# Performance work log

Hardware: AMD Instinct MI355X
Metric: run time of the kernel (lower is better)

Reference implementation:

```python
import jax, jax.numpy as jnp
import numpy as np

SPATIAL = [(56, 100), (28, 50), (14, 25), (7, 13)]
L_TOT = sum(h * w for h, w in SPATIAL)  # 7441
IMG_H, IMG_W = 448.0, 800.0
HH, NLEV, NPTS = 8, 4, 4
C, FFN = 256, 1024
PC = [-54.0, -54.0, -5.0, 54.0, 54.0, 3.0]
GRID_XY = 1080 // 8


def mlp2(x, w1, b1, w2, b2):
    return jnp.maximum(x @ w1 + b1, 0.0) @ w2 + b2


def ln(x):
    m = x.mean(-1, keepdims=True)
    v = ((x - m) ** 2).mean(-1, keepdims=True)
    return (x - m) * jax.lax.rsqrt(v + 1e-5)


def bilinear_sample(feat, loc):
    # feat [h,w,D]; loc [N,2] normalized to [0,1]; zero padding, align_corners=False
    h, w = feat.shape[0], feat.shape[1]
    x = loc[:, 0] * w - 0.5
    y = loc[:, 1] * h - 0.5
    x0f = jnp.floor(x); y0f = jnp.floor(y)
    wx = (x - x0f)[:, None]; wy = (y - y0f)[:, None]
    x0 = x0f.astype(jnp.int32); y0 = y0f.astype(jnp.int32)
    def g(xi, yi):
        inb = ((xi >= 0) & (xi < w) & (yi >= 0) & (yi < h))[:, None]
        return feat[jnp.clip(yi, 0, h - 1), jnp.clip(xi, 0, w - 1)] * inb
    return (g(x0, y0) * (1 - wx) * (1 - wy) + g(x0 + 1, y0) * wx * (1 - wy)
            + g(x0, y0 + 1) * (1 - wx) * wy + g(x0 + 1, y0 + 1) * wx * wy)


def setup_inputs() -> dict:
    key = jax.random.key(0)
    ks = jax.random.split(key, 40)
    B, V, P = 4, 6, 200
    f = jnp.float32
    def w(i, shape, s=0.05):
        return jax.random.normal(ks[i], shape, f) * s
    inp = {
        'img_query_feat': jax.random.normal(ks[1], (B, C, P), f),
        'img_query_pos': jax.random.uniform(ks[2], (B, P, 3), dtype=f),
        'img_query_view_mask': jax.random.randint(ks[3], (B, P, V), 0, 2).astype(jnp.int32),
        'img_feats_stack': jax.random.normal(ks[4], (B, V, C, L_TOT), f),
        'normal_img_feats_pos_stack': jax.random.normal(ks[5], (L_TOT, 2), f),
        'lidar2img_rt': jnp.eye(4, dtype=f) + 0.01 * jax.random.normal(ks[0], (B, V, 4, 4), f),
        'lidar2cam_r': jnp.broadcast_to(jnp.eye(3, dtype=f), (B, V, 3, 3)) + 0.01 * jax.random.normal(ks[6], (B, V, 3, 3), f),
        'lidar2cam_t': jax.random.normal(ks[7], (B, V, 3), f),
        'qpos_w1': w(8, (3, C)), 'qpos_b1': jnp.zeros((C,), f),
        'qpos_w2': w(9, (C, C)), 'qpos_b2': jnp.zeros((C,), f),
        'kpos_w1': w(10, (6, C)), 'kpos_b1': jnp.zeros((C,), f),
        'kpos_w2': w(11, (C, C)), 'kpos_b2': jnp.zeros((C,), f),
        'sa_wq': w(12, (C, C)), 'sa_wk': w(13, (C, C)),
        'sa_wv': w(14, (C, C)), 'sa_wo': w(15, (C, C)),
        'dv_w': w(16, (C, C)),
        'doff_w': w(17, (C, HH * NLEV * NPTS * 2)), 'doff_b': jnp.zeros((HH * NLEV * NPTS * 2,), f),
        'dattn_w': w(18, (C, HH * NLEV * NPTS)), 'dattn_b': jnp.zeros((HH * NLEV * NPTS,), f),
        'dout_w': w(19, (C, C)),
        'ffn_w1': w(20, (C, FFN)), 'ffn_b1': jnp.zeros((FFN,), f),
        'ffn_w2': w(21, (FFN, C)), 'ffn_b2': jnp.zeros((C,), f),
        'pred_w1': w(22, (C, C)), 'pred_b1': jnp.zeros((C,), f),
        'pred_w2': w(23, (C, 3)), 'pred_b2': jnp.zeros((3,), f),
    }
    return inp


def reference(img_query_feat, img_query_pos, img_query_view_mask, img_feats_stack,
              normal_img_feats_pos_stack, lidar2img_rt, lidar2cam_r, lidar2cam_t,
              qpos_w1, qpos_b1, qpos_w2, qpos_b2, kpos_w1, kpos_b1, kpos_w2, kpos_b2,
              sa_wq, sa_wk, sa_wv, sa_wo, dv_w, doff_w, doff_b, dattn_w, dattn_b, dout_w,
              ffn_w1, ffn_b1, ffn_w2, ffn_b2, pred_w1, pred_b1, pred_w2, pred_b2):
    B, V, _, L = img_feats_stack.shape
    P = img_query_feat.shape[-1]
    Dh = C // HH

    # key 3D positions: denormalize -> backproject via inv(lidar2img) -> append cam center
    pos2d = jax.nn.sigmoid(normal_img_feats_pos_stack) * jnp.array([IMG_W, IMG_H], jnp.float32)
    pos4 = jnp.concatenate([pos2d, jnp.ones((L, 2), pos2d.dtype)], -1)  # [L,4]
    inv_rt = jnp.linalg.inv(lidar2img_rt)                               # [B,V,4,4]
    key3d = jnp.einsum('bvij,lj->bvli', inv_rt, pos4)[..., :3]          # [B,V,L,3]
    cam_t = -jnp.einsum('bvji,bvj->bvi', lidar2cam_r, lidar2cam_t)      # [B,V,3]
    key_pos6 = jnp.concatenate([key3d, jnp.broadcast_to(cam_t[:, :, None], key3d.shape)], -1)
    kpos_emb = mlp2(key_pos6, kpos_w1, kpos_b1, kpos_w2, kpos_b2)       # [B,V,L,C]
    qpos_emb = mlp2(img_query_pos, qpos_w1, qpos_b1, qpos_w2, qpos_b2)  # [B,P,C]

    # per-view normalized reference points from lidar->image projection
    qpad = jnp.concatenate([img_query_pos, jnp.ones((B, P, 1), img_query_pos.dtype)], -1)
    proj = jnp.einsum('bvij,bpj->bvpi', lidar2img_rt, qpad)
    ref = (proj[..., :2] / proj[..., 2:3]) / jnp.array([IMG_W, IMG_H], jnp.float32)  # [B,V,P,2]

    # on-image mask; views with <=1 query are skipped (as in original)
    mv = jnp.transpose(img_query_view_mask > 0, (0, 2, 1))  # [B,V,P]
    mv = mv & (mv.sum(-1, keepdims=True) > 1)

    # self attention among on-image queries (shared qkv, per-view key mask)
    x = jnp.transpose(img_query_feat, (0, 2, 1))  # [B,P,C]
    xq = x + qpos_emb
    q = (xq @ sa_wq).reshape(B, P, HH, Dh)
    k = (xq @ sa_wk).reshape(B, P, HH, Dh)
    v = (x @ sa_wv).reshape(B, P, HH, Dh)
    logits = jnp.einsum('bqhd,bkhd->bhqk', q, k) / np.sqrt(Dh).astype(np.float32)
    logits = logits[:, None] + jnp.where(mv[:, :, None, None, :], 0.0, -1e9)  # [B,V,HH,P,P]
    attn = jax.nn.softmax(logits, axis=-1)
    sa = jnp.einsum('bvhqk,bkhd->bvqhd', attn, v).reshape(B, V, P, C) @ sa_wo
    x1 = ln(x[:, None] + sa)  # [B,V,P,C]

    # multi-scale deformable cross attention
    vals = ((jnp.transpose(img_feats_stack, (0, 1, 3, 2)) + kpos_emb) @ dv_w).reshape(B, V, L, HH, Dh)
    q2 = x1 + qpos_emb[:, None]
    off = (q2 @ doff_w + doff_b).reshape(B, V, P, HH, NLEV, NPTS, 2)
    aw = jax.nn.softmax((q2 @ dattn_w + dattn_b).reshape(B, V, P, HH, NLEV * NPTS), -1)
    aw = aw.reshape(B, V, P, HH, NLEV, NPTS)
    wh = jnp.array([[float(w_), float(h_)] for (h_, w_) in SPATIAL], jnp.float32)  # [NLEV,2]
    loc = ref[:, :, :, None, None, None, :] + off / wh[:, None, :]
    out = jnp.zeros((B, V, P, HH, Dh), x.dtype)
    start = 0
    for l, (h_, w_) in enumerate(SPATIAL):
        feat_l = vals[:, :, start:start + h_ * w_]
        start += h_ * w_
        feat_l = jnp.transpose(feat_l.reshape(B, V, h_, w_, HH, Dh), (0, 1, 4, 2, 3, 5)).reshape(B * V * HH, h_, w_, Dh)
        loc_l = jnp.transpose(loc[:, :, :, :, l], (0, 1, 3, 2, 4, 5)).reshape(B * V * HH, P * NPTS, 2)
        s = jax.vmap(bilinear_sample)(feat_l, loc_l).reshape(B, V, HH, P, NPTS, Dh)
        out = out + jnp.einsum('bvhpnd,bvphn->bvphd', s, aw[:, :, :, :, l])
    x2 = ln(x1 + out.reshape(B, V, P, C) @ dout_w)
    x3 = ln(x2 + mlp2(x2, ffn_w1, ffn_b1, ffn_w2, ffn_b2))  # [B,V,P,C]

    # masked scatter-accumulate across views, count-normalized
    mk = mv[..., None].astype(x.dtype)            # [B,V,P,1]
    fused = (x3 * mk).sum(1) / (mk.sum(1) + 1e-4)  # [B,P,C]
    img_query_feat_out = jnp.transpose(fused, (0, 2, 1))

    # prediction head: center refinement + BEV normalization
    center = mlp2(fused, pred_w1, pred_b1, pred_w2, pred_b2) + img_query_pos  # [B,P,3]
    img_query_pos_out = jax.lax.stop_gradient(center)
    cx = (center[..., 0] - PC[0]) / (PC[3] - PC[0]) * GRID_XY
    cy = (center[..., 1] - PC[1]) / (PC[4] - PC[1]) * GRID_XY
    center_bev = jnp.stack([cx, cy], -1)
    img_query_pos_bev = jax.lax.stop_gradient(center_bev)
    height = jnp.transpose(center[..., 2:3], (0, 2, 1))
    center_out = jnp.transpose(center_bev, (0, 2, 1))
    return img_query_feat_out, img_query_pos_out, img_query_pos_bev, center_out, height
```

## Files before the change

### kernel.cpp

```cpp
#include <hip/hip_runtime.h>
#include <hip/hip_bf16.h>
#include <cstdint>
#include <cstddef>

using bf16 = __hip_bfloat16;
#define DEVFN static __device__ __forceinline__

constexpr int B = 4, V = 6, P = 200, C = 256, HH = 8, Dh = 32, NLEV = 4, NPTS = 4, FFN = 1024;
constexpr int L = 7441;
constexpr int BV = B * V, BP = B * P, BVP = B * V * P, BVL = B * V * L;
constexpr float IMG_W = 800.f, IMG_H = 448.f;

__constant__ int cLH[4] = {56, 28, 14, 7};
__constant__ int cLW[4] = {100, 50, 25, 13};
__constant__ int cLS[4] = {0, 5600, 7000, 7350};

constexpr size_t IRT   = 0;
constexpr size_t CAMT  = IRT + (size_t)BV * 16;
constexpr size_t MFLAG = CAMT + (size_t)BV * 3;
constexpr size_t Xo    = MFLAG + BV;
constexpr size_t QPOSo = Xo + (size_t)BP * C;
constexpr size_t Qo    = QPOSo + (size_t)BP * C;
constexpr size_t Ko    = Qo + (size_t)BP * C;
constexpr size_t VVo   = Ko + (size_t)BP * C;
constexpr size_t LOGo  = VVo + (size_t)BP * C;
constexpr size_t SAo   = LOGo + (size_t)B * HH * P * P;
constexpr size_t X1o   = SAo + (size_t)BVP * C;
constexpr size_t REFo  = X1o + (size_t)BVP * C;
constexpr size_t OFFo  = REFo + (size_t)BVP * 2;
constexpr size_t AWo   = OFFo + (size_t)BVP * 256;
constexpr size_t OUTSo = AWo + (size_t)BVP * 128;
constexpr size_t X2o   = OUTSo + (size_t)BVP * C;
constexpr size_t X3o   = X2o + (size_t)BVP * C;
constexpr size_t FUSEDo= X3o + (size_t)BVP * C;
constexpr size_t B2DVo = FUSEDo + (size_t)BP * C;
constexpr size_t WS_FLOATS = B2DVo + 256;
constexpr size_t VALS_BYTE_OFF = ((WS_FLOATS * 4 + 255) / 256) * 256;
constexpr size_t VALS_ELEMS = (size_t)BVL * C;

constexpr size_t KW2NB_O = 0;
constexpr size_t DVWT_O  = 65536;
constexpr size_t WOT_O   = 131072;
constexpr size_t DOUTT_O = 196608;
constexpr size_t OAWT_O  = 262144;
constexpr size_t QKVT_O  = 360448;
constexpr size_t W1T_O   = 753664;
constexpr size_t W2T_O   = 1015808;
constexpr size_t HIDB_O  = 1277952;
constexpr size_t KDVT_O  = HIDB_O;

constexpr size_t O0 = 0;
constexpr size_t O1 = O0 + (size_t)B * C * P;
constexpr size_t O2 = O1 + (size_t)B * P * 3;
constexpr size_t O3 = O2 + (size_t)B * P * 2;
constexpr size_t O4 = O3 + (size_t)B * 2 * P;

DEVFN float tof(bf16 x) { return __bfloat162float(x); }
DEVFN bf16  tobf(float x) { return __float2bfloat16(x); }

typedef __attribute__((ext_vector_type(8))) short short8;
typedef __attribute__((ext_vector_type(4))) float floatx4;

DEVFN float blockReduceSum(float v, float* red) {
    int j = threadIdx.x;
    __syncthreads();
    red[j] = v; __syncthreads();
    for (int s = 128; s > 0; s >>= 1) { if (j < s) red[j] += red[j + s]; __syncthreads(); }
    return red[0];
}

DEVFN float dotK(const float* __restrict__ s, const float* __restrict__ W, int j, int N, int K) {
    float acc = 0.f;
    for (int k = 0; k < K; k += 4) {
        float4 h = *(const float4*)(s + k);
        acc += h.x * W[(size_t)(k + 0) * N + j];
        acc += h.y * W[(size_t)(k + 1) * N + j];
        acc += h.z * W[(size_t)(k + 2) * N + j];
        acc += h.w * W[(size_t)(k + 3) * N + j];
    }
    return acc;
}

__global__ __launch_bounds__(64) void k_setup(const float* rt, const float* l2cr, const float* l2ct,
                                              const int* maskin, float* ws) {
    int t = threadIdx.x;
    if (t >= BV) return;
    float m[16], inv[16];
    for (int i = 0; i < 16; i++) m[i] = rt[t * 16 + i];
    inv[0]  =  m[5]*m[10]*m[15] - m[5]*m[11]*m[14] - m[9]*m[6]*m[15] + m[9]*m[7]*m[14] + m[13]*m[6]*m[11] - m[13]*m[7]*m[10];
    inv[4]  = -m[4]*m[10]*m[15] + m[4]*m[11]*m[14] + m[8]*m[6]*m[15] - m[8]*m[7]*m[14] - m[12]*m[6]*m[11] + m[12]*m[7]*m[10];
    inv[8]  =  m[4]*m[9]*m[15]  - m[4]*m[11]*m[13] - m[8]*m[5]*m[15] + m[8]*m[7]*m[13] + m[12]*m[5]*m[11] - m[12]*m[7]*m[9];
    inv[12] = -m[4]*m[9]*m[14]  + m[4]*m[10]*m[13] + m[8]*m[5]*m[14] - m[8]*m[6]*m[13] - m[12]*m[5]*m[10] + m[12]*m[6]*m[9];
    inv[1]  = -m[1]*m[10]*m[15] + m[1]*m[11]*m[14] + m[9]*m[2]*m[15] - m[9]*m[3]*m[14] - m[13]*m[2]*m[11] + m[13]*m[3]*m[10];
    inv[5]  =  m[0]*m[10]*m[15] - m[0]*m[11]*m[14] - m[8]*m[2]*m[15] + m[8]*m[3]*m[14] + m[12]*m[2]*m[11] - m[12]*m[3]*m[10];
    inv[9]  = -m[0]*m[9]*m[15]  + m[0]*m[11]*m[13] + m[8]*m[1]*m[15] - m[8]*m[3]*m[13] - m[12]*m[1]*m[11] + m[12]*m[3]*m[9];
    inv[13] =  m[0]*m[9]*m[14]  - m[0]*m[10]*m[13] - m[8]*m[1]*m[14] + m[8]*m[2]*m[13] + m[12]*m[1]*m[10] - m[12]*m[2]*m[9];
    inv[2]  =  m[1]*m[6]*m[15]  - m[1]*m[7]*m[14]  - m[5]*m[2]*m[15] + m[5]*m[3]*m[14] + m[13]*m[2]*m[7]  - m[13]*m[3]*m[6];
    inv[6]  = -m[0]*m[6]*m[15]  + m[0]*m[7]*m[14]  + m[4]*m[2]*m[15] - m[4]*m[3]*m[14] - m[12]*m[2]*m[7]  + m[12]*m[3]*m[6];
    inv[10] =  m[0]*m[5]*m[15]  - m[0]*m[7]*m[13]  - m[4]*m[1]*m[15] + m[4]*m[3]*m[13] + m[12]*m[1]*m[7]  - m[12]*m[3]*m[5];
    inv[14] = -m[0]*m[5]*m[14]  + m[0]*m[6]*m[13]  + m[4]*m[1]*m[14] - m[4]*m[2]*m[13] - m[12]*m[1]*m[6]  + m[12]*m[2]*m[5];
    inv[3]  = -m[1]*m[6]*m[11]  + m[1]*m[7]*m[10]  + m[5]*m[2]*m[11] - m[5]*m[3]*m[10] - m[9]*m[2]*m[7]   + m[9]*m[3]*m[6];
    inv[7]  =  m[0]*m[6]*m[11]  - m[0]*m[7]*m[10]  - m[4]*m[2]*m[11] + m[4]*m[3]*m[10] + m[8]*m[2]*m[7]   - m[8]*m[3]*m[6];
    inv[11] = -m[0]*m[5]*m[11]  + m[0]*m[7]*m[9]   + m[4]*m[1]*m[11] - m[4]*m[3]*m[9]  - m[8]*m[1]*m[7]   + m[8]*m[3]*m[5];
    inv[15] =  m[0]*m[5]*m[10]  - m[0]*m[6]*m[9]   - m[4]*m[1]*m[10] + m[4]*m[2]*m[9]  + m[8]*m[1]*m[6]   - m[8]*m[2]*m[5];
    float det = m[0]*inv[0] + m[1]*inv[4] + m[2]*inv[8] + m[3]*inv[12];
    float rd = 1.f / det;
    for (int i = 0; i < 16; i++) ws[IRT + t * 16 + i] = inv[i] * rd;
    float r9[9], tv[3];
    for (int i = 0; i < 9; i++) r9[i] = l2cr[t * 9 + i];
    for (int i = 0; i < 3; i++) tv[i] = l2ct[t * 3 + i];
    for (int i = 0; i < 3; i++)
        ws[CAMT + t * 3 + i] = -(r9[0 * 3 + i] * tv[0] + r9[1 * 3 + i] * tv[1] + r9[2 * 3 + i] * tv[2]);
    int b = t / V, v = t % V, cnt = 0;
    for (int p = 0; p < P; p++) cnt += (maskin[(b * P + p) * V + v] > 0) ? 1 : 0;
    ws[MFLAG + t] = (cnt > 1) ? 1.f : 0.f;
}

__global__ __launch_bounds__(256) void k_wprep_all(
        const float* kw2, const float* dvw, const float* wo, const float* dw,
        const float* offw, const float* attw, const float* wq, const float* wk, const float* wv,
        const float* w1, const float* w2, bf16* wb) {
    int bid = blockIdx.x, t = threadIdx.x;
    if (bid < 1024) {
        int reg = bid >> 8, n = bid & 255;
        if (reg == 0) {
            wb[(size_t)n * 256 + t] = tobf(kw2[(size_t)n * 256 + t]);
        } else {
            const float* src = (reg == 1) ? dvw : (reg == 2) ? wo : dw;
            wb[(size_t)reg * 65536 + (size_t)n * 256 + t] = tobf(src[(size_t)t * 256 + n]);
        }
    } else if (bid < 1408) {
        int n = bid - 1024;
        float v = (n < 256) ? offw[(size_t)t * 256 + n] : attw[(size_t)t * 128 + (n - 256)];
        wb[OAWT_O + (size_t)n * 256 + t] = tobf(v);
    } else if (bid < 2176) {
        int n = bid - 1408;
        bf16* dst = wb + QKVT_O + (size_t)n * 512;
        float v0 = (n < 256) ? wq[(size_t)t * 256 + n] : (n < 512) ? wk[(size_t)t * 256 + (n - 256)]
                                                                   : wv[(size_t)t * 256 + (n - 512)];
        dst[t] = tobf(v0);
        float v1 = (n < 256) ? wq[(size_t)t * 256 + n] : (n < 512) ? wk[(size_t)t * 256 + (n - 256)] : 0.f;
        dst[t + 256] = tobf(v1);
    } else if (bid < 3200) {
        int n = bid - 2176;
        wb[W1T_O + (size_t)n * 256 + t] = tobf(w1[(size_t)t * 1024 + n]);
    } else {
        int n = bid - 3200;
        bf16* dst = wb + W2T_O + (size_t)n * 1024;
        for (int kk = 0; kk < 4; kk++)
            dst[t + kk * 256] = tobf(w2[(size_t)(t + kk * 256) * 256 + n]);
    }
}

constexpr int GAST = 264;
__global__ __launch_bounds__(256) void k_wfuse(const bf16* __restrict__ dvwT, const bf16* __restrict__ kw2nb,
                                               const float* __restrict__ b2, bf16* __restrict__ kdvT,
                                               float* ws) {
    __shared__ __align__(16) bf16 As[32 * GAST];
    int row0 = blockIdx.x * 32;
    int t = threadIdx.x;
    for (int rr = 0; rr < 32; rr++)
        As[rr * GAST + t] = dvwT[(size_t)(row0 + rr) * 256 + t];
    __syncthreads();
    int wave = t >> 6, lane = t & 63, quad = lane >> 4, l15 = lane & 15;
    int n0 = wave * 64;
    floatx4 acc[2][4];
    #pragma unroll
    for (int i = 0; i < 2; i++)
        #pragma unroll
        for (int nt = 0; nt < 4; nt++) acc[i][nt] = (floatx4){0.f, 0.f, 0.f, 0.f};
    for (int kk = 0; kk < 8; kk++) {
        short8 a0 = *(const short8*)&As[l15 * GAST + kk * 32 + quad * 8];
        short8 a1 = *(const short8*)&As[(16 + l15) * GAST + kk * 32 + quad * 8];
        #pragma unroll
        for (int nt = 0; nt < 4; nt++) {
            short8 bf = *(const short8*)&kw2nb[(size_t)(n0 + nt * 16 + l15) * 256 + kk * 32 + quad * 8];
            acc[0][nt] = __builtin_amdgcn_mfma_f32_16x16x32_bf16(a0, bf, acc[0][nt], 0, 0, 0);
            acc[1][nt] = __builtin_amdgcn_mfma_f32_16x16x32_bf16(a1, bf, acc[1][nt], 0, 0, 0);
        }
    }
    #pragma unroll
    for (int i = 0; i < 2; i++)
        #pragma unroll
        for (int nt = 0; nt < 4; nt++) {
            int col = n0 + nt * 16 + l15;
            int rl = i * 16 + quad * 4;
            #pragma unroll
            for (int u = 0; u < 4; u++)
                kdvT[(size_t)(row0 + rl + u) * 256 + col] = tobf(acc[i][nt][u]);
        }
    {
        int r = t >> 3, pp = t & 7;
        float s = 0.f;
        for (int n = pp * 32; n < pp * 32 + 32; n++)
            s += tof(As[r * GAST + n]) * b2[n];
        s += __shfl_down(s, 4, 8);
        s += __shfl_down(s, 2, 8);
        s += __shfl_down(s, 1, 8);
        if (pp == 0) ws[B2DVo + row0 + r] = s;
    }
}

__global__ __launch_bounds__(256) void k_qpos(const float* qfeat, const float* qposin,
                                              const float* w1, const float* b1, const float* w2, const float* b2,
                                              float* ws) {
    int row = blockIdx.x, j = threadIdx.x;
    int b = row / P, p = row % P;
    __shared__ __align__(16) float pos[4];
    __shared__ __align__(16) float hid[C];
    if (j < 3) pos[j] = qposin[row * 3 + j];
    __syncthreads();
    float h = b1[j] + pos[0] * w1[0 * C + j] + pos[1] * w1[1 * C + j] + pos[2] * w1[2 * C + j];
    hid[j] = fmaxf(h, 0.f);
    __syncthreads();
    float acc = b2[j] + dotK(hid, w2, j, C, C);
    ws[QPOSo + (size_t)row * C + j] = acc;
    ws[Xo + (size_t)row * C + j] = qfeat[((size_t)b * C + j) * P + p];
}

constexpr int AST2 = 520;
__global__ __launch_bounds__(256) void k_qkv_mfma(const bf16* __restrict__ qkvT, float* ws) {
    __shared__ __align__(16) bf16 As[16 * AST2];
    int row0 = blockIdx.x * 16;
    int t = threadIdx.x;
    for (int rr = 0; rr < 16; rr++) {
        As[rr * AST2 + t]       = tobf(ws[Xo + (size_t)(row0 + rr) * C + t]);
        As[rr * AST2 + 256 + t] = tobf(ws[QPOSo + (size_t)(row0 + rr) * C + t]);
    }
    __syncthreads();
    int wave = t >> 6, lane = t & 63, quad = lane >> 4, l15 = lane & 15;
    int n0 = wave * 192;
    floatx4 acc[12];
    #pragma unroll
    for (int nt = 0; nt < 12; nt++) acc[nt] = (floatx4){0.f, 0.f, 0.f, 0.f};
    for (int kk = 0; kk < 16; kk++) {
        short8 a = *(const short8*)&As[l15 * AST2 + kk * 32 + quad * 8];
        #pragma unroll
        for (int nt = 0; nt < 12; nt++) {
            short8 bf = *(const short8*)&qkvT[(size_t)(n0 + nt * 16 + l15) * 512 + kk * 32 + quad * 8];
            acc[nt] = __builtin_amdgcn_mfma_f32_16x16x32_bf16(a, bf, acc[nt], 0, 0, 0);
        }
    }
    #pragma unroll
    for (int nt = 0; nt < 12; nt++) {
        int n = n0 + nt * 16 + l15;
        int which = n >> 8, c = n & 255;
        size_t dst = (which == 0) ? Qo : (which == 1) ? Ko : VVo;
        int row = row0 + quad * 4;
        #pragma unroll
        for (int u = 0; u < 4; u++)
            ws[dst + (size_t)(row + u) * C + c] = acc[nt][u];
    }
}

__global__ __launch_bounds__(256) void k_logits(float* ws) {
    int bid = blockIdx.x;
    int qi = bid % P, h = (bid / P) % HH, b = bid / (P * HH);
    int j = threadIdx.x;
    __shared__ __align__(16) float qf[Dh];
    if (j < Dh) qf[j] = ws[Qo + ((size_t)(b * P + qi)) * C + h * Dh + j];
    __syncthreads();
    if (j < P) {
        const float* kp = ws + Ko + ((size_t)(b * P + j)) * C + h * Dh;
        float acc = 0.f;
        for (int d = 0; d < Dh; d += 4) {
            float4 kv = *(const float4*)(kp + d);
            float4 qv = *(const float4*)(qf + d);
            acc += kv.x * qv.x + kv.y * qv.y + kv.z * qv.z + kv.w * qv.w;
        }
        ws[LOGo + (size_t)bid * P + j] = acc * 0.17677669529663687f;
    }
}

__global__ __launch_bounds__(256) void k_sattn(const int* maskin, float* ws) {
    int bid = blockIdx.x;
    int qi = bid % P, h = (bid / P) % HH, v = (bid / (P * HH)) % V, b = bid / (P * HH * V);
    int j = threadIdx.x;
    __shared__ float attn[256];
    __shared__ float red[256];
    __shared__ float rw[8];
    float flag = ws[MFLAG + b * V + v];
    float val = -1e30f;
    if (j < P) {
        float lg = ws[LOGo + ((size_t)(b * HH + h) * P + qi) * P + j];
        bool mk = (flag > 0.5f) && (maskin[(b * P + j) * V + v] > 0);
        val = lg + (mk ? 0.f : -1e9f);
    }
    int wv = j >> 6;
    float m = val;
    #pragma unroll
    for (int off = 32; off > 0; off >>= 1) m = fmaxf(m, __shfl_xor(m, off, 64));
    if ((j & 63) == 0) rw[wv] = m;
    __syncthreads();
    m = fmaxf(fmaxf(rw[0], rw[1]), fmaxf(rw[2], rw[3]));
    float e = (j < P) ? __expf(val - m) : 0.f;
    float s = e;
    #pragma unroll
    for (int off = 32; off > 0; off >>= 1) s += __shfl_xor(s, off, 64);
    if ((j & 63) == 0) rw[4 + wv] = s;
    __syncthreads();
    s = (rw[4] + rw[5]) + (rw[6] + rw[7]);
    attn[j] = e / s;
    __syncthreads();
    int d = j & 31, c = j >> 5;
    const float* vvp = ws + VVo + (size_t)b * P * C + h * Dh + d;
    float acc = 0.f;
    for (int kk = c * 25; kk < c * 25 + 25; ++kk) acc += attn[kk] * vvp[(size_t)kk * C];
    red[j] = acc; __syncthreads();
    if (j < Dh) {
        float s2 = 0.f;
        for (int c2 = 0; c2 < 8; c2++) s2 += red[c2 * 32 + j];
        ws[SAo + ((size_t)((b * V + v) * P + qi)) * C + h * Dh + j] = s2;
    }
}

constexpr int OST = 260;
__global__ __launch_bounds__(256) void k_lngemm(const bf16* __restrict__ WT,
        float* ws, size_t aOff, size_t residOff, int residMode, size_t dstOff) {
    __shared__ __align__(16) bf16 As[32 * GAST];
    __shared__ __align__(16) float Os[32 * OST];
    __shared__ float redw[4][8][2];
    __shared__ float mv[8][2];
    int row0 = blockIdx.x * 32;
    int t = threadIdx.x;
    for (int rr = 0; rr < 32; rr++)
        As[rr * GAST + t] = tobf(ws[aOff + (size_t)(row0 + rr) * C + t]);
    __syncthreads();
    int wave = t >> 6, lane = t & 63, quad = lane >> 4, l15 = lane & 15;
    int n0 = wave * 64;
    floatx4 acc[2][4];
    #pragma unroll
    for (int i = 0; i < 2; i++)
        #pragma unroll
        for (int nt = 0; nt < 4; nt++) acc[i][nt] = (floatx4){0.f, 0.f, 0.f, 0.f};
    for (int kk = 0; kk < 8; kk++) {
        short8 a0 = *(const short8*)&As[l15 * GAST + kk * 32 + quad * 8];
        short8 a1 = *(const short8*)&As[(16 + l15) * GAST + kk * 32 + quad * 8];
        #pragma unroll
        for (int nt = 0; nt < 4; nt++) {
            short8 bf = *(const short8*)&WT[(size_t)(n0 + nt * 16 + l15) * 256 + kk * 32 + quad * 8];
            acc[0][nt] = __builtin_amdgcn_mfma_f32_16x16x32_bf16(a0, bf, acc[0][nt], 0, 0, 0);
            acc[1][nt] = __builtin_amdgcn_mfma_f32_16x16x32_bf16(a1, bf, acc[1][nt], 0, 0, 0);
        }
    }
    #pragma unroll
    for (int i = 0; i < 2; i++)
        #pragma unroll
        for (int nt = 0; nt < 4; nt++) {
            int col = n0 + nt * 16 + l15;
            int rl = i * 16 + quad * 4;
            #pragma unroll
            for (int u = 0; u < 4; u++) Os[(rl + u) * OST + col] = acc[i][nt][u];
        }
    __syncthreads();
    int lane2 = t & 63, wv = t >> 6;
    for (int g = 0; g < 4; g++) {
        float rv[8];
        #pragma unroll
        for (int r = 0; r < 8; r++) {
            int grow = row0 + g * 8 + r;
            int ridx = residMode ? ((grow / (P * V)) * P + grow % P) : grow;
            rv[r] = Os[(g * 8 + r) * OST + t] + ws[residOff + (size_t)ridx * C + t];
        }
        #pragma unroll
        for (int r = 0; r < 8; r++) {
            float s = rv[r], q = rv[r] * rv[r];
            for (int off = 32; off > 0; off >>= 1) {
                s += __shfl_down(s, off, 64);
                q += __shfl_down(q, off, 64);
            }
            if (lane2 == 0) { redw[wv][r][0] = s; redw[wv][r][1] = q; }
        }
        __syncthreads();
        if (t < 8) {
            float s = redw[0][t][0] + redw[1][t][0] + redw[2][t][0] + redw[3][t][0];
            float q = redw[0][t][1] + redw[1][t][1] + redw[2][t][1] + redw[3][t][1];
            float mean = s * (1.f / C);
            float var = q * (1.f / C) - mean * mean;
            mv[t][0] = mean; mv[t][1] = rsqrtf(var + 1e-5f);
        }
        __syncthreads();
        #pragma unroll
        for (int r = 0; r < 8; r++) {
            int grow = row0 + g * 8 + r;
            ws[dstOff + (size_t)grow * C + t] = (rv[r] - mv[r][0]) * mv[r][1];
        }
        __syncthreads();
    }
}

__global__ __launch_bounds__(256) void k_ref(const float* qposin, const float* rt, float* ws) {
    int tid = blockIdx.x * 256 + threadIdx.x;
    if (tid >= BVP) return;
    int p = tid % P, v = (tid / P) % V, b = tid / (P * V);
    float p0 = qposin[(b * P + p) * 3 + 0];
    float p1 = qposin[(b * P + p) * 3 + 1];
    float p2 = qposin[(b * P + p) * 3 + 2];
    const float* m = rt + (size_t)(b * V + v) * 16;
    float pr[3];
    for (int i = 0; i < 3; i++)
        pr[i] = m[i * 4 + 0] * p0 + m[i * 4 + 1] * p1 + m[i * 4 + 2] * p2 + m[i * 4 + 3];
    ws[REFo + (size_t)tid * 2 + 0] = pr[0] / pr[2] / IMG_W;
    ws[REFo + (size_t)tid * 2 + 1] = pr[1] / pr[2] / IMG_H;
}

constexpr int OAWST = 392;
__global__ __launch_bounds__(256) void k_offaw_mfma(const bf16* __restrict__ oawT,
        const float* __restrict__ ob, const float* __restrict__ ab, float* ws) {
    __shared__ __align__(16) bf16 As[32 * GAST];
    __shared__ __align__(16) float Os[32 * OAWST];
    int row0 = blockIdx.x * 32;
    int t = threadIdx.x;
    for (int rr = 0; rr < 32; rr++) {
        int grow = row0 + rr;
        int ridx = (grow / (P * V)) * P + grow % P;
        As[rr * GAST + t] = tobf(ws[X1o + (size_t)grow * C + t] + ws[QPOSo + (size_t)ridx * C + t]);
    }
    __syncthreads();
    int wave = t >> 6, lane = t & 63, quad = lane >> 4, l15 = lane & 15;
    int n0 = wave * 96;
    floatx4 acc[2][6];
    #pragma unroll
    for (int i = 0; i < 2; i++)
        #pragma unroll
        for (int nt = 0; nt < 6; nt++) acc[i][nt] = (floatx4){0.f, 0.f, 0.f, 0.f};
    for (int kk = 0; kk < 8; kk++) {
        short8 a0 = *(const short8*)&As[l15 * GAST + kk * 32 + quad * 8];
        short8 a1 = *(const short8*)&As[(16 + l15) * GAST + kk * 32 + quad * 8];
        #pragma unroll
        for (int nt = 0; nt < 6; nt++) {
            short8 bf = *(const short8*)&oawT[(size_t)(n0 + nt * 16 + l15) * 256 + kk * 32 + quad * 8];
            acc[0][nt] = __builtin_amdgcn_mfma_f32_16x16x32_bf16(a0, bf, acc[0][nt], 0, 0, 0);
            acc[1][nt] = __builtin_amdgcn_mfma_f32_16x16x32_bf16(a1, bf, acc[1][nt], 0, 0, 0);
        }
    }
    #pragma unroll
    for (int i = 0; i < 2; i++)
        #pragma unroll
        for (int nt = 0; nt < 6; nt++) {
            int col = n0 + nt * 16 + l15;
            int rl = i * 16 + quad * 4;
            #pragma unroll
            for (int u = 0; u < 4; u++) Os[(rl + u) * OAWST + col] = acc[i][nt][u];
        }
    __syncthreads();
    float obv = ob[t];
    for (int r = 0; r < 32; r++)
        ws[OFFo + (size_t)(row0 + r) * 256 + t] = Os[r * OAWST + t] + obv;
    {
        int r = t >> 3, g = t & 7;
        const float* lg = &Os[r * OAWST + 256 + g * 16];
        float mx = -1e30f;
        #pragma unroll
        for (int i = 0; i < 16; i++) mx = fmaxf(mx, lg[i] + ab[g * 16 + i]);
        float s = 0.f;
        float ex[16];
        #pragma unroll
        for (int i = 0; i < 16; i++) { ex[i] = __expf(lg[i] + ab[g * 16 + i] - mx); s += ex[i]; }
        float rs = 1.f / s;
        #pragma unroll
        for (int i = 0; i < 16; i++)
            ws[AWo + (size_t)(row0 + r) * 128 + g * 16 + i] = ex[i] * rs;
    }
}

constexpr int VROWS = 64;
constexpr int ASTR = C + 8;
constexpr int NVT = (L + VROWS - 1) / VROWS;

DEVFN int swidx(int r, int c) {
    return r * ASTR + ((c & 7) | ((((c >> 3) ^ ((r >> 3) & 7))) << 3));
}
DEVFN int swblk(int r, int cb) {
    return r * ASTR + (((cb ^ ((r >> 3) & 7))) << 3);
}

__global__ __launch_bounds__(256, 4) void k_vals_mfma(
        const float* __restrict__ npos, const float* __restrict__ feats,
        const float* __restrict__ kw1, const float* __restrict__ kb1,
        const bf16* __restrict__ kdvT, const bf16* __restrict__ dvwT,
        const float* __restrict__ ws, bf16* __restrict__ vals) {
    __shared__ __align__(16) bf16 As[VROWS * ASTR];
    __shared__ float kp6s[VROWS][8];
    __shared__ float b2s[C];
    int bv = blockIdx.y;
    int l0 = blockIdx.x * VROWS;
    int t = threadIdx.x;
    bool full = (l0 + VROWS <= L);

    float4 fb1[8];
    if (full) {
        #pragma unroll
        for (int rnd = 0; rnd < 8; rnd++) {
            int c = rnd * 16 + (t >> 4), ql = (t & 15) * 4;
            fb1[rnd] = *(const float4*)&feats[((size_t)bv * C + c) * L + l0 + ql];
        }
    }
    b2s[t] = ws[B2DVo + t];
    if (t < VROWS) {
        int l = min(l0 + t, L - 1);
        float sx = 1.f / (1.f + __expf(-npos[l * 2 + 0])) * IMG_W;
        float sy = 1.f / (1.f + __expf(-npos[l * 2 + 1])) * IMG_H;
        const float* inv = ws + IRT + (size_t)bv * 16;
        #pragma unroll
        for (int i = 0; i < 3; i++)
            kp6s[t][i] = inv[i * 4 + 0] * sx + inv[i * 4 + 1] * sy + inv[i * 4 + 2] + inv[i * 4 + 3];
        #pragma unroll
        for (int i = 0; i < 3; i++) kp6s[t][3 + i] = ws[CAMT + (size_t)bv * 3 + i];
    }
    __syncthreads();
    {
        float w1j[6];
        #pragma unroll
        for (int i = 0; i < 6; i++) w1j[i] = kw1[i * C + t];
        float bb = kb1[t];
        for (int r = 0; r < VROWS; r++) {
            float h = bb;
            #pragma unroll
            for (int i = 0; i < 6; i++) h += kp6s[r][i] * w1j[i];
            As[swidx(r, t)] = tobf(fmaxf(h, 0.f));
        }
    }
    __syncthreads();
    int wave = t >> 6, lane = t & 63;
    int quad = lane >> 4, l15 = lane & 15;
    int mh = (wave >> 1) * 32;
    int nh = (wave & 1) * 128;
    floatx4 acc[2][8];
    #pragma unroll
    for (int i = 0; i < 2; i++)
        #pragma unroll
        for (int nt = 0; nt < 8; nt++) acc[i][nt] = (floatx4){0.f, 0.f, 0.f, 0.f};
    for (int kk = 0; kk < 8; kk++) {
        short8 a0 = *(const short8*)&As[swblk(mh + l15, kk * 4 + quad)];
        short8 a1 = *(const short8*)&As[swblk(mh + 16 + l15, kk * 4 + quad)];
        #pragma unroll
        for (int nt = 0; nt < 8; nt++) {
            short8 bfr = *(const short8*)&kdvT[(size_t)(nh + nt * 16 + l15) * C + kk * 32 + quad * 8];
            acc[0][nt] = __builtin_amdgcn_mfma_f32_16x16x32_bf16(a0, bfr, acc[0][nt], 0, 0, 0);
            acc[1][nt] = __builtin_amdgcn_mfma_f32_16x16x32_bf16(a1, bfr, acc[1][nt], 0, 0, 0);
        }
    }
    __syncthreads();
    if (full) {
        float4 fb2[8];
        #pragma unroll
        for (int rnd = 0; rnd < 8; rnd++) {
            int c = 128 + rnd * 16 + (t >> 4), ql = (t & 15) * 4;
            fb2[rnd] = *(const float4*)&feats[((size_t)bv * C + c) * L + l0 + ql];
        }
        #pragma unroll
        for (int rnd = 0; rnd < 8; rnd++) {
            int c = rnd * 16 + (t >> 4), ql = (t & 15) * 4;
            As[swidx(ql + 0, c)] = tobf(fb1[rnd].x);
            As[swidx(ql + 1, c)] = tobf(fb1[rnd].y);
            As[swidx(ql + 2, c)] = tobf(fb1[rnd].z);
            As[swidx(ql + 3, c)] = tobf(fb1[rnd].w);
        }
        #pragma unroll
        for (int rnd = 0; rnd < 8; rnd++) {
            int c = 128 + rnd * 16 + (t >> 4), ql = (t & 15) * 4;
            As[swidx(ql + 0, c)] = tobf(fb2[rnd].x);
            As[swidx(ql + 1, c)] = tobf(fb2[rnd].y);
            As[swidx(ql + 2, c)] = tobf(fb2[rnd].z);
            As[swidx(ql + 3, c)] = tobf(fb2[rnd].w);
        }
    } else {
        for (int rnd = 0; rnd < 16; rnd++) {
            int c = rnd * 16 + (t >> 4), ql = (t & 15) * 4;
            size_t fbase = ((size_t)bv * C + c) * L + l0 + ql;
            #pragma unroll
            for (int u = 0; u < 4; u++) {
                float fv = (l0 + ql + u < L) ? feats[fbase + u] : 0.f;
                As[swidx(ql + u, c)] = tobf(fv);
            }
        }
    }
    __syncthreads();
    for (int kk = 0; kk < 8; kk++) {
        short8 a0 = *(const short8*)&As[swblk(mh + l15, kk * 4 + quad)];
        short8 a1 = *(const short8*)&As[swblk(mh + 16 + l15, kk * 4 + quad)];
        #pragma unroll
        for (int nt = 0; nt < 8; nt++) {
            short8 bfr = *(const short8*)&dvwT[(size_t)(nh + nt * 16 + l15) * C + kk * 32 + quad * 8];
            acc[0][nt] = __builtin_amdgcn_mfma_f32_16x16x32_bf16(a0, bfr, acc[0][nt], 0, 0, 0);
            acc[1][nt] = __builtin_amdgcn_mfma_f32_16x16x32_bf16(a1, bfr, acc[1][nt], 0, 0, 0);
        }
    }
    __syncthreads();
    #pragma unroll
    for (int i = 0; i < 2; i++) {
        #pragma unroll
        for (int nt = 0; nt < 8; nt++) {
            int c = nh + nt * 16 + l15;
            int rb = mh + i * 16 + quad * 4;
            float bias = b2s[c];
            #pragma unroll
            for (int u = 0; u < 4; u++)
                As[swidx(rb + u, c)] = tobf(acc[i][nt][u] + bias);
        }
    }
    __syncthreads();
    #pragma unroll
    for (int pass = 0; pass < 8; pass++) {
        int row = pass * 8 + (t >> 5);
        int cb = t & 31;
        int l = l0 + row;
        if (l < L)
            *(int4*)&vals[((size_t)bv * L + l) * C + cb * 8] = *(const int4*)&As[swblk(row, cb)];
    }
}

__global__ __launch_bounds__(256) void k_sample(const float* ws, const bf16* vals, float* wsmut) {
    int bid0 = blockIdx.x;
    int row = (bid0 & 7) * (BVP / 8) + (bid0 >> 3);
    int j = threadIdx.x;
    int h = j >> 5, d = j & 31;
    __shared__ float soff[256];
    __shared__ float sawL[128];
    __shared__ float sref[2];
    soff[j] = ws[OFFo + (size_t)row * 256 + j];
    if (j < 128) sawL[j] = ws[AWo + (size_t)row * 128 + j];
    if (j < 2) sref[j] = ws[REFo + (size_t)row * 2 + j];
    __syncthreads();
    int v = (row / P) % V, b = row / (P * V);
    const bf16* vbase = vals + (size_t)(b * V + v) * L * C + h * Dh + d;
    float acc = 0.f;
    for (int l = 0; l < NLEV; l++) {
        float Wf = (float)cLW[l], Hf = (float)cLH[l];
        int Wi = cLW[l], Hi = cLH[l], S0 = cLS[l];
        for (int n = 0; n < NPTS; n++) {
            int oi = ((h * NLEV + l) * NPTS + n) * 2;
            float lx = sref[0] + soff[oi + 0] / Wf;
            float ly = sref[1] + soff[oi + 1] / Hf;
            float aww = sawL[(h * NLEV + l) * NPTS + n];
            float x = lx * Wf - 0.5f, y = ly * Hf - 0.5f;
            float x0f = floorf(x), y0f = floorf(y);
            float wx = x - x0f, wy = y - y0f;
            int x0 = (int)x0f, y0 = (int)y0f;
            float s = 0.f;
            #pragma unroll
            for (int dy = 0; dy < 2; dy++) {
                #pragma unroll
                for (int dx = 0; dx < 2; dx++) {
                    int xi = x0 + dx, yi = y0 + dy;
                    if (xi >= 0 && xi < Wi && yi >= 0 && yi < Hi) {
                        float wwt = (dx ? wx : 1.f - wx) * (dy ? wy : 1.f - wy);
                        s += wwt * tof(vbase[(size_t)(S0 + yi * Wi + xi) * C]);
                    }
                }
            }
            acc += aww * s;
        }
    }
    wsmut[OUTSo + (size_t)row * C + j] = acc;
}

__global__ __launch_bounds__(256) void k_ffn1(const bf16* __restrict__ w1T, const float* __restrict__ b1,
                                              float* ws, bf16* hidb) {
    __shared__ __align__(16) bf16 As[32 * GAST];
    __shared__ __align__(16) bf16 Hs[32 * AST2];
    int row0 = blockIdx.x * 32;
    int nb = blockIdx.y * 512;
    int t = threadIdx.x;
    for (int rr = 0; rr < 32; rr++)
        As[rr * GAST + t] = tobf(ws[X2o + (size_t)(row0 + rr) * C + t]);
    __syncthreads();
    int wave = t >> 6, lane = t & 63, quad = lane >> 4, l15 = lane & 15;
    int n0 = wave * 128;
    floatx4 acc[2][8];
    #pragma unroll
    for (int i = 0; i < 2; i++)
        #pragma unroll
        for (int nt = 0; nt < 8; nt++) acc[i][nt] = (floatx4){0.f, 0.f, 0.f, 0.f};
    for (int kk = 0; kk < 8; kk++) {
        short8 a0 = *(const short8*)&As[l15 * GAST + kk * 32 + quad * 8];
        short8 a1 = *(const short8*)&As[(16 + l15) * GAST + kk * 32 + quad * 8];
        #pragma unroll
        for (int nt = 0; nt < 8; nt++) {
            short8 bf = *(const short8*)&w1T[(size_t)(nb + n0 + nt * 16 + l15) * 256 + kk * 32 + quad * 8];
            acc[0][nt] = __builtin_amdgcn_mfma_f32_16x16x32_bf16(a0, bf, acc[0][nt], 0, 0, 0);
            acc[1][nt] = __builtin_amdgcn_mfma_f32_16x16x32_bf16(a1, bf, acc[1][nt], 0, 0, 0);
        }
    }
    #pragma unroll
    for (int i = 0; i < 2; i++)
        #pragma unroll
        for (int nt = 0; nt < 8; nt++) {
            int cl = n0 + nt * 16 + l15;
            float bias = b1[nb + cl];
            int rl = i * 16 + quad * 4;
            #pragma unroll
            for (int u = 0; u < 4; u++)
                Hs[(rl + u) * AST2 + cl] = tobf(fmaxf(acc[i][nt][u] + bias, 0.f));
        }
    __syncthreads();
    #pragma unroll
    for (int pass = 0; pass < 8; pass++) {
        int row = pass * 4 + (t >> 6);
        int col = (t & 63) * 8;
        *(int4*)&hidb[(size_t)(row0 + row) * FFN + nb + col] = *(const int4*)&Hs[row * AST2 + col];
    }
}

__global__ __launch_bounds__(256) void k_ffn2(const bf16* __restrict__ w2T, const float* __restrict__ b2,
                                              const bf16* __restrict__ hidb, float* ws) {
    __shared__ __align__(16) float Os[32 * OST];
    __shared__ float redw[4][8][2];
    __shared__ float mv[8][2];
    int row0 = blockIdx.x * 32;
    int t = threadIdx.x;
    int wave = t >> 6, lane = t & 63, quad = lane >> 4, l15 = lane & 15;
    int n0 = wave * 64;
    floatx4 acc[2][4];
    #pragma unroll
    for (int i = 0; i < 2; i++)
        #pragma unroll
        for (int nt = 0; nt < 4; nt++) acc[i][nt] = (floatx4){0.f, 0.f, 0.f, 0.f};
    for (int kk = 0; kk < 32; kk++) {
        short8 a0 = *(const short8*)&hidb[(size_t)(row0 + l15) * FFN + kk * 32 + quad * 8];
        short8 a1 = *(const short8*)&hidb[(size_t)(row0 + 16 + l15) * FFN + kk * 32 + quad * 8];
        #pragma unroll
        for (int nt = 0; nt < 4; nt++) {
            short8 bf = *(const short8*)&w2T[(size_t)(n0 + nt * 16 + l15) * FFN + kk * 32 + quad * 8];
            acc[0][nt] = __builtin_amdgcn_mfma_f32_16x16x32_bf16(a0, bf, acc[0][nt], 0, 0, 0);
            acc[1][nt] = __builtin_amdgcn_mfma_f32_16x16x32_bf16(a1, bf, acc[1][nt], 0, 0, 0);
        }
    }
    #pragma unroll
    for (int i = 0; i < 2; i++)
        #pragma unroll
        for (int nt = 0; nt < 4; nt++) {
            int col = n0 + nt * 16 + l15;
            float bias = b2[col];
            int rl = i * 16 + quad * 4;
            #pragma unroll
            for (int u = 0; u < 4; u++) Os[(rl + u) * OST + col] = acc[i][nt][u] + bias;
        }
    __syncthreads();
    for (int g = 0; g < 4; g++) {
        float rv[8];
        #pragma unroll
        for (int r = 0; r < 8; r++) {
            int grow = row0 + g * 8 + r;
            rv[r] = Os[(g * 8 + r) * OST + t] + ws[X2o + (size_t)grow * C + t];
        }
        #pragma unroll
        for (int r = 0; r < 8; r++) {
            float s = rv[r], q = rv[r] * rv[r];
            for (int off = 32; off > 0; off >>= 1) {
                s += __shfl_down(s, off, 64);
                q += __shfl_down(q, off, 64);
            }
            if (lane == 0) { redw[wave][r][0] = s; redw[wave][r][1] = q; }
        }
        __syncthreads();
        if (t < 8) {
            float s = redw[0][t][0] + redw[1][t][0] + redw[2][t][0] + redw[3][t][0];
            float q = redw[0][t][1] + redw[1][t][1] + redw[2][t][1] + redw[3][t][1];
            float mean = s * (1.f / C);
            float var = q * (1.f / C) - mean * mean;
            mv[t][0] = mean; mv[t][1] = rsqrtf(var + 1e-5f);
        }
        __syncthreads();
        #pragma unroll
        for (int r = 0; r < 8; r++) {
            int grow = row0 + g * 8 + r;
            ws[X3o + (size_t)grow * C + t] = (rv[r] - mv[r][0]) * mv[r][1];
        }
        __syncthreads();
    }
}

__global__ __launch_bounds__(256) void k_fuse(const int* maskin, float* ws, float* out) {
    int row = blockIdx.x, j = threadIdx.x;
    int b = row / P, p = row % P;
    float s = 0.f, cnt = 0.f;
    for (int v = 0; v < V; v++) {
        bool mk = (maskin[(b * P + p) * V + v] > 0) && (ws[MFLAG + b * V + v] > 0.5f);
        if (mk) {
            s += ws[X3o + ((size_t)((b * V + v) * P + p)) * C + j];
            cnt += 1.f;
        }
    }
    float f = s / (cnt + 1e-4f);
    ws[FUSEDo + (size_t)row * C + j] = f;
    out[O0 + ((size_t)b * C + j) * P + p] = f;
}

__global__ __launch_bounds__(256) void k_pred(const float* w1, const float* b1, const float* w2, const float* b2,
                                              const float* qposin, float* ws, float* out) {
    int row = blockIdx.x, j = threadIdx.x;
    __shared__ __align__(16) float in[C];
    __shared__ float red[256];
    __shared__ float cen[4];
    in[j] = ws[FUSEDo + (size_t)row * C + j];
    __syncthreads();
    float h = fmaxf(b1[j] + dotK(in, w1, j, C, C), 0.f);
    for (int i = 0; i < 3; i++) {
        float s = blockReduceSum(h * w2[j * 3 + i], red);
        if (j == 0) cen[i] = s + b2[i] + qposin[row * 3 + i];
    }
    if (j == 0) {
        float c0 = cen[0], c1 = cen[1], c2 = cen[2];
        float cx = (c0 + 54.f) / 108.f * 135.f;
        float cy = (c1 + 54.f) / 108.f * 135.f;
        int b = row / P, p = row % P;
        out[O1 + (size_t)row * 3 + 0] = c0;
        out[O1 + (size_t)row * 3 + 1] = c1;
        out[O1 + (size_t)row * 3 + 2] = c2;
        out[O2 + (size_t)row * 2 + 0] = cx;
        out[O2 + (size_t)row * 2 + 1] = cy;
        out[O3 + (size_t)b * 2 * P + 0 * P + p] = cx;
        out[O3 + (size_t)b * 2 * P + 1 * P + p] = cy;
        out[O4 + (size_t)b * P + p] = c2;
    }
}

extern "C" void kernel_launch(void* const* d_in, const int* in_sizes, int n_in,
                              void* d_out, int out_size, void* d_ws, size_t ws_size,
                              hipStream_t stream) {
    const float* qfeat  = (const float*)d_in[0];
    const float* qposin = (const float*)d_in[1];
    const int*   maskin = (const int*)d_in[2];
    const float* feats  = (const float*)d_in[3];
    const float* npos   = (const float*)d_in[4];
    const float* rt     = (const float*)d_in[5];
    const float* l2cr   = (const float*)d_in[6];
    const float* l2ct   = (const float*)d_in[7];
    const float* qp_w1 = (const float*)d_in[8],  * qp_b1 = (const float*)d_in[9];
    const float* qp_w2 = (const float*)d_in[10], * qp_b2 = (const float*)d_in[11];
    const float* kp_w1 = (const float*)d_in[12], * kp_b1 = (const float*)d_in[13];
    const float* kp_w2 = (const float*)d_in[14], * kp_b2 = (const float*)d_in[15];
    const float* sa_wq = (const float*)d_in[16], * sa_wk = (const float*)d_in[17];
    const float* sa_wv = (const float*)d_in[18];
    const float* sa_wo = (const float*)d_in[19];
    const float* dv_w  = (const float*)d_in[20];
    const float* doffw = (const float*)d_in[21], * doffb = (const float*)d_in[22];
    const float* dattw = (const float*)d_in[23], * dattb = (const float*)d_in[24];
    const float* doutw = (const float*)d_in[25];
    const float* f_w1  = (const float*)d_in[26], * f_b1 = (const float*)d_in[27];
    const float* f_w2  = (const float*)d_in[28], * f_b2 = (const float*)d_in[29];
    const float* p_w1  = (const float*)d_in[30], * p_b1 = (const float*)d_in[31];
    const float* p_w2  = (const float*)d_in[32], * p_b2 = (const float*)d_in[33];

    float* ws = (float*)d_ws;
    bf16* vals = (bf16*)((char*)d_ws + VALS_BYTE_OFF);
    bf16* wb = vals + VALS_ELEMS;
    bf16* hidb = wb + HIDB_O;
    float* out = (float*)d_out;

    k_setup<<<1, 64, 0, stream>>>(rt, l2cr, l2ct, maskin, ws);
    k_wprep_all<<<3456, 256, 0, stream>>>(kp_w2, dv_w, sa_wo, doutw, doffw, dattw,
                                          sa_wq, sa_wk, sa_wv, f_w1, f_w2, wb);
    k_wfuse<<<8, 256, 0, stream>>>(wb + DVWT_O, wb + KW2NB_O, kp_b2, wb + KDVT_O, ws);
    k_qpos<<<BP, 256, 0, stream>>>(qfeat, qposin, qp_w1, qp_b1, qp_w2, qp_b2, ws);
    k_qkv_mfma<<<BP / 16, 256, 0, stream>>>(wb + QKVT_O, ws);
    k_logits<<<B * HH * P, 256, 0, stream>>>(ws);
    k_sattn<<<B * V * HH * P, 256, 0, stream>>>(maskin, ws);
    k_lngemm<<<BVP / 32, 256, 0, stream>>>(wb + WOT_O, ws, SAo, Xo, 1, X1o);
    k_ref<<<(BVP + 255) / 256, 256, 0, stream>>>(qposin, rt, ws);
    k_offaw_mfma<<<BVP / 32, 256, 0, stream>>>(wb + OAWT_O, doffb, dattb, ws);
    k_vals_mfma<<<dim3(NVT, BV), 256, 0, stream>>>(npos, feats, kp_w1, kp_b1,
                                                   wb + KDVT_O, wb + DVWT_O, ws, vals);
    k_sample<<<BVP, 256, 0, stream>>>(ws, vals, ws);
    k_lngemm<<<BVP / 32, 256, 0, stream>>>(wb + DOUTT_O, ws, OUTSo, X1o, 0, X2o);
    k_ffn1<<<dim3(BVP / 32, 2), 256, 0, stream>>>(wb + W1T_O, f_b1, ws, hidb);
    k_ffn2<<<BVP / 32, 256, 0, stream>>>(wb + W2T_O, f_b2, hidb, ws);
    k_fuse<<<BP, 256, 0, stream>>>(maskin, ws, out);
    k_pred<<<BP, 256, 0, stream>>>(p_w1, p_b1, p_w2, p_b2, qposin, ws, out);
}
```

Baseline: 871.6 us.

## Batch all views per block in self-attention and drop feats register prefetch

Measured after the change: 866.4 us. No clear change (-0.6%).

```diff
diff --git a/kernel.cpp b/kernel.cpp
--- a/kernel.cpp
+++ b/kernel.cpp
@@ -274,43 +274,67 @@
 
 __global__ __launch_bounds__(256) void k_sattn(const int* maskin, float* ws) {
     int bid = blockIdx.x;
-    int qi = bid % P, h = (bid / P) % HH, v = (bid / (P * HH)) % V, b = bid / (P * HH * V);
+    int qi = bid % P, h = (bid / P) % HH, b = bid / (P * HH);
     int j = threadIdx.x;
-    __shared__ float attn[256];
-    __shared__ float red[256];
-    __shared__ float rw[8];
-    float flag = ws[MFLAG + b * V + v];
-    float val = -1e30f;
-    if (j < P) {
-        float lg = ws[LOGo + ((size_t)(b * HH + h) * P + qi) * P + j];
-        bool mk = (flag > 0.5f) && (maskin[(b * P + j) * V + v] > 0);
-        val = lg + (mk ? 0.f : -1e9f);
-    }
+    __shared__ float attn[V][256];
+    __shared__ float red6[V * 8 * 32];
+    __shared__ float rwm[V][4], rws[V][4];
     int wv = j >> 6;
-    float m = val;
-    #pragma unroll
-    for (int off = 32; off > 0; off >>= 1) m = fmaxf(m, __shfl_xor(m, off, 64));
-    if ((j & 63) == 0) rw[wv] = m;
-    __syncthreads();
-    m = fmaxf(fmaxf(rw[0], rw[1]), fmaxf(rw[2], rw[3]));
-    float e = (j < P) ? __expf(val - m) : 0.f;
-    float s = e;
-    #pragma unroll
-    for (int off = 32; off > 0; off >>= 1) s += __shfl_xor(s, off, 64);
-    if ((j & 63) == 0) rw[4 + wv] = s;
-    __syncthreads();
-    s = (rw[4] + rw[5]) + (rw[6] + rw[7]);
-    attn[j] = e / s;
+    float lg = (j < P) ? ws[LOGo + ((size_t)(b * HH + h) * P + qi) * P + j] : 0.f;
+    float val[V];
+    #pragma unroll
+    for (int v = 0; v < V; v++) {
+        bool mk = false;
+        if (j < P) {
+            float flag = ws[MFLAG + b * V + v];
+            mk = (flag > 0.5f) && (maskin[(b * P + j) * V + v] > 0);
+        }
+        val[v] = (j < P) ? (lg + (mk ? 0.f : -1e9f)) : -1e30f;
+    }
+    #pragma unroll
+    for (int v = 0; v < V; v++) {
+        float m = val[v];
+        #pragma unroll
+        for (int off = 32; off > 0; off >>= 1) m = fmaxf(m, __shfl_xor(m, off, 64));
+        if ((j & 63) == 0) rwm[v][wv] = m;
+    }
+    __syncthreads();
+    float ee[V];
+    #pragma unroll
+    for (int v = 0; v < V; v++) {
+        float m = fmaxf(fmaxf(rwm[v][0], rwm[v][1]), fmaxf(rwm[v][2], rwm[v][3]));
+        ee[v] = (j < P) ? __expf(val[v] - m) : 0.f;
+        float s = ee[v];
+        #pragma unroll
+        for (int off = 32; off > 0; off >>= 1) s += __shfl_xor(s, off, 64);
+        if ((j & 63) == 0) rws[v][wv] = s;
+    }
+    __syncthreads();
+    #pragma unroll
+    for (int v = 0; v < V; v++) {
+        float s = (rws[v][0] + rws[v][1]) + (rws[v][2] + rws[v][3]);
+        attn[v][j] = ee[v] / s;
+    }
     __syncthreads();
     int d = j & 31, c = j >> 5;
     const float* vvp = ws + VVo + (size_t)b * P * C + h * Dh + d;
-    float acc = 0.f;
-    for (int kk = c * 25; kk < c * 25 + 25; ++kk) acc += attn[kk] * vvp[(size_t)kk * C];
-    red[j] = acc; __syncthreads();
-    if (j < Dh) {
+    float acc[V];
+    #pragma unroll
+    for (int v = 0; v < V; v++) acc[v] = 0.f;
+    for (int kk = c * 25; kk < c * 25 + 25; ++kk) {
+        float vv = vvp[(size_t)kk * C];
+        #pragma unroll
+        for (int v = 0; v < V; v++) acc[v] += attn[v][kk] * vv;
+    }
+    #pragma unroll
+    for (int v = 0; v < V; v++) red6[(v * 8 + c) * 32 + d] = acc[v];
+    __syncthreads();
+    if (j < V * 32) {
+        int v = j >> 5, dd = j & 31;
         float s2 = 0.f;
-        for (int c2 = 0; c2 < 8; c2++) s2 += red[c2 * 32 + j];
-        ws[SAo + ((size_t)((b * V + v) * P + qi)) * C + h * Dh + j] = s2;
+        #pragma unroll
+        for (int c2 = 0; c2 < 8; c2++) s2 += red6[(v * 8 + c2) * 32 + dd];
+        ws[SAo + ((size_t)((b * V + v) * P + qi)) * C + h * Dh + dd] = s2;
     }
 }
 
@@ -488,14 +512,6 @@
     int t = threadIdx.x;
     bool full = (l0 + VROWS <= L);
 
-    float4 fb1[8];
-    if (full) {
-        #pragma unroll
-        for (int rnd = 0; rnd < 8; rnd++) {
-            int c = rnd * 16 + (t >> 4), ql = (t & 15) * 4;
-            fb1[rnd] = *(const float4*)&feats[((size_t)bv * C + c) * L + l0 + ql];
-        }
-    }
     b2s[t] = ws[B2DVo + t];
     if (t < VROWS) {
         int l = min(l0 + t, L - 1);
@@ -543,31 +559,20 @@
     }
     __syncthreads();
     if (full) {
-        float4 fb2[8];
-        #pragma unroll
-        for (int rnd = 0; rnd < 8; rnd++) {
-            int c = 128 + rnd * 16 + (t >> 4), ql = (t & 15) * 4;
-            fb2[rnd] = *(const float4*)&feats[((size_t)bv * C + c) * L + l0 + ql];
-        }
-        #pragma unroll
-        for (int rnd = 0; rnd < 8; rnd++) {
-            int c = rnd * 16 + (t >> 4), ql = (t & 15) * 4;
-            As[swidx(ql + 0, c)] = tobf(fb1[rnd].x);
-            As[swidx(ql + 1, c)] = tobf(fb1[rnd].y);
-            As[swidx(ql + 2, c)] = tobf(fb1[rnd].z);
-            As[swidx(ql + 3, c)] = tobf(fb1[rnd].w);
-        }
-        #pragma unroll
-        for (int rnd = 0; rnd < 8; rnd++) {
-            int c = 128 + rnd * 16 + (t >> 4), ql = (t & 15) * 4;
-            As[swidx(ql + 0, c)] = tobf(fb2[rnd].x);
-            As[swidx(ql + 1, c)] = tobf(fb2[rnd].y);
-            As[swidx(ql + 2, c)] = tobf(fb2[rnd].z);
-            As[swidx(ql + 3, c)] = tobf(fb2[rnd].w);
+        #pragma unroll
+        for (int rnd = 0; rnd < 16; rnd++) {
+            int q = rnd * 256 + t;
+            int c = q >> 4, ql = (q & 15) * 4;
+            float4 f = *(const float4*)&feats[((size_t)bv * C + c) * L + l0 + ql];
+            As[swidx(ql + 0, c)] = tobf(f.x);
+            As[swidx(ql + 1, c)] = tobf(f.y);
+            As[swidx(ql + 2, c)] = tobf(f.z);
+            As[swidx(ql + 3, c)] = tobf(f.w);
         }
     } else {
         for (int rnd = 0; rnd < 16; rnd++) {
-            int c = rnd * 16 + (t >> 4), ql = (t & 15) * 4;
+            int q = rnd * 256 + t;
+            int c = q >> 4, ql = (q & 15) * 4;
             size_t fbase = ((size_t)bv * C + c) * L + l0 + ql;
             #pragma unroll
             for (int u = 0; u < 4; u++) {
@@ -857,7 +862,7 @@
     k_qpos<<<BP, 256, 0, stream>>>(qfeat, qposin, qp_w1, qp_b1, qp_w2, qp_b2, ws);
     k_qkv_mfma<<<BP / 16, 256, 0, stream>>>(wb + QKVT_O, ws);
     k_logits<<<B * HH * P, 256, 0, stream>>>(ws);
-    k_sattn<<<B * V * HH * P, 256, 0, stream>>>(maskin, ws);
+    k_sattn<<<B * HH * P, 256, 0, stream>>>(maskin, ws);
     k_lngemm<<<BVP / 32, 256, 0, stream>>>(wb + WOT_O, ws, SAo, Xo, 1, X1o);
     k_ref<<<(BVP + 255) / 256, 256, 0, stream>>>(qposin, rt, ws);
     k_offaw_mfma<<<BVP / 32, 256, 0, stream>>>(wb + OAWT_O, doffb, dattb, ws);
```
